# Kernel optimization log

Measured on AMD Instinct MI355X. Metric: run time of the kernel, lower is better.

## Reference

```python
import jax, jax.numpy as jnp
import numpy as np

DIM = 2048
N_HEADS = 16
N_KV_HEADS = 4
HEAD_DIM = DIM // N_HEADS


def setup_inputs() -> dict:
    key = jax.random.key(0)
    k1, k2, k3, k4, k5 = jax.random.split(key, 5)
    B, T = 2, 2048
    scale = 1.0 / np.sqrt(DIM)
    x = jax.random.normal(k1, (B, T, DIM), dtype=jnp.float32)
    # weights stored as [in, out] so forward is x @ W (same math as nn.Linear)
    Wq = jax.random.normal(k2, (DIM, DIM), dtype=jnp.float32) * scale
    Wk = jax.random.normal(k3, (DIM, N_KV_HEADS * HEAD_DIM), dtype=jnp.float32) * scale
    Wv = jax.random.normal(k4, (DIM, N_KV_HEADS * HEAD_DIM), dtype=jnp.float32) * scale
    Wo = jax.random.normal(k5, (DIM, DIM), dtype=jnp.float32) * scale
    return {"x": x, "Wq": Wq, "Wk": Wk, "Wv": Wv, "Wo": Wo}


def reference(x, Wq, Wk, Wv, Wo):
    B, T, C = x.shape
    G = N_HEADS // N_KV_HEADS  # query heads per kv head
    # projections
    q = (x @ Wq).reshape(B, T, N_KV_HEADS, G, HEAD_DIM)   # [B,T,K,G,d]
    k = (x @ Wk).reshape(B, T, N_KV_HEADS, HEAD_DIM)      # [B,T,K,d]
    v = (x @ Wv).reshape(B, T, N_KV_HEADS, HEAD_DIM)      # [B,T,K,d]
    # attention scores: grouped heads share kv head (no repeat_interleave copy)
    att = jnp.einsum('btkgd,bskd->bkgts', q, k) / np.sqrt(HEAD_DIM)  # [B,K,G,T,T]
    att = jax.nn.softmax(att, axis=-1)
    out = jnp.einsum('bkgts,bskd->btkgd', att, v).reshape(B, T, C)
    return out @ Wo
```

## Files before the change

### kernel.cpp

```cpp
#include <hip/hip_runtime.h>
#include <hip/hip_bf16.h>

typedef __hip_bfloat16 bf16;
typedef __attribute__((ext_vector_type(8))) short short8;
typedef __attribute__((ext_vector_type(4))) short short4v;
typedef __attribute__((ext_vector_type(4))) float f32x4;

#define DIMC 2048
#define TSEQ 2048
#define NB 2
#define KVH 4
#define NH 16
#define HD 128
#define KVD 512
#define QSCALE 0.12751744f

__device__ __forceinline__ void mfma16(f32x4& acc, short8 a, short8 b) {
  acc = __builtin_amdgcn_mfma_f32_16x16x32_bf16(a, b, acc, 0, 0, 0);
}

__device__ __forceinline__ void gload_lds16(const bf16* g, bf16* l) {
  __builtin_amdgcn_global_load_lds(
      (const __attribute__((address_space(1))) void*)g,
      (__attribute__((address_space(3))) void*)l, 16, 0, 0);
}

__device__ __forceinline__ int swz(int row, int col) {
  return col ^ ((row & 7) << 3);
}

__global__ __launch_bounds__(256) void f2b(const float* __restrict__ in,
                                           bf16* __restrict__ out, long n4) {
  long i = (long)blockIdx.x * 256 + threadIdx.x;
  if (i >= n4) return;
  const f32x4 v = *(const f32x4*)(in + i * 4);
  union { short4v s; bf16 h[4]; } u;
#pragma unroll
  for (int j = 0; j < 4; ++j) u.h[j] = __float2bfloat16(v[j]);
  *(short4v*)(out + i * 4) = u.s;
}

__global__ __launch_bounds__(256) void transpose_all(const float* __restrict__ Wq,
                                                     const float* __restrict__ Wk,
                                                     const float* __restrict__ Wv,
                                                     const float* __restrict__ Wo,
                                                     bf16* __restrict__ WT3,
                                                     bf16* __restrict__ WoT) {
  __shared__ bf16 tile[64][72];
  const int y = blockIdx.y;
  const float* in;
  bf16* out;
  int C, rb, cb;
  float scale = 1.0f;
  if (y < 32) {
    in = Wq; out = WT3; C = 2048;
    rb = y * 64; cb = blockIdx.x * 64; scale = QSCALE;
  } else if (y < 40) {
    in = Wk; out = WT3 + (long)2048 * DIMC; C = 512;
    rb = blockIdx.x * 64; cb = (y - 32) * 64;
  } else if (y < 48) {
    in = Wv; out = WT3 + (long)2560 * DIMC; C = 512;
    rb = blockIdx.x * 64; cb = (y - 40) * 64;
  } else {
    in = Wo; out = WoT; C = 2048;
    rb = (y - 48) * 64; cb = blockIdx.x * 64;
  }
  int tx = threadIdx.x & 63, ty = threadIdx.x >> 6;
  for (int i = ty; i < 64; i += 4)
    tile[i][tx] = __float2bfloat16(in[(long)(rb + i) * C + cb + tx] * scale);
  __syncthreads();
  for (int i = ty; i < 64; i += 4)
    out[(long)(cb + i) * DIMC + rb + tx] = tile[tx][i];
}

#define GEMM_BODY(A_, Bt_, K_)                                                  \
  const int tid = threadIdx.x;                                                  \
  const int lane = tid & 63, wid = tid >> 6;                                    \
  const long m0 = blockIdx.y * 128, n0 = blockIdx.x * 128;                      \
  const int wm = (wid >> 1) * 64, wn = (wid & 1) * 64;                          \
  f32x4 acc[4][4] = {};                                                         \
  const int srow = lane >> 2, scol = (lane & 3) * 8;                            \
  const bf16* Ag = A_ + (m0 + srow) * (long)K_ + scol;                          \
  const bf16* Bg = Bt_ + (n0 + srow) * (long)K_ + scol;                         \
  for (int k0 = 0; k0 < K_; k0 += 32) {                                         \
    for (int p = 0; p < 2; ++p) {                                               \
      int rr = p * 64 + wid * 16;                                               \
      gload_lds16(Ag + (long)rr * K_ + k0, As + rr * 32);                       \
      gload_lds16(Bg + (long)rr * K_ + k0, Bs + rr * 32);                       \
    }                                                                           \
    __syncthreads();                                                            \
    const int ko = (lane >> 4) * 8;                                             \
    short8 af[4], bq[4];                                                        \
    _Pragma("unroll") for (int i = 0; i < 4; ++i) {                             \
      af[i] = *(const short8*)(As + (wm + i * 16 + (lane & 15)) * 32 + ko);     \
      bq[i] = *(const short8*)(Bs + (wn + i * 16 + (lane & 15)) * 32 + ko);     \
    }                                                                           \
    _Pragma("unroll") for (int i = 0; i < 4; ++i)                               \
      _Pragma("unroll") for (int j = 0; j < 4; ++j)                             \
        mfma16(acc[i][j], af[i], bq[j]);                                        \
    __syncthreads();                                                            \
  }                                                                             \
  const int cr = (lane >> 4) * 4, cc = lane & 15;

__global__ __launch_bounds__(256) void gemm_qkv(const bf16* __restrict__ A,
                                                const bf16* __restrict__ Bt,
                                                bf16* __restrict__ qp,
                                                bf16* __restrict__ kp,
                                                bf16* __restrict__ vT) {
  __shared__ bf16 As[128 * 32];
  __shared__ bf16 Bs[128 * 32];
  GEMM_BODY(A, Bt, 2048)
#pragma unroll
  for (int i = 0; i < 4; ++i)
#pragma unroll
    for (int j = 0; j < 4; ++j)
#pragma unroll
      for (int r = 0; r < 4; ++r) {
        long m = m0 + wm + i * 16 + cr + r;
        long n = n0 + wn + j * 16 + cc;
        float val = acc[i][j][r];
        if (n0 < 2048) {
          qp[m * DIMC + n] = __float2bfloat16(val);
        } else if (n0 < 2560) {
          kp[m * KVD + (n - 2048)] = __float2bfloat16(val);
        } else {
          long nn = n - 2560;
          long z = (m >> 11) * 4 + (nn >> 7);
          vT[z * (HD * (long)TSEQ) + (nn & 127) * (long)TSEQ + (m & 2047)] =
              __float2bfloat16(val);
        }
      }
}

__global__ __launch_bounds__(256) void gemm_out(const bf16* __restrict__ A,
                                                const bf16* __restrict__ Bt,
                                                float* __restrict__ C) {
  __shared__ bf16 As[128 * 32];
  __shared__ bf16 Bs[128 * 32];
  GEMM_BODY(A, Bt, 2048)
#pragma unroll
  for (int i = 0; i < 4; ++i)
#pragma unroll
    for (int j = 0; j < 4; ++j)
#pragma unroll
      for (int r = 0; r < 4; ++r) {
        long m = m0 + wm + i * 16 + cr + r;
        long n = n0 + wn + j * 16 + cc;
        C[m * DIMC + n] = acc[i][j][r];
      }
}

__global__ __launch_bounds__(512, 2) void attn_fwd(const bf16* __restrict__ Qp,
                                                   const bf16* __restrict__ Kp,
                                                   const bf16* __restrict__ Vt,
                                                   bf16* __restrict__ AO) {
  __shared__ bf16 Ks[2][64 * 128];
  __shared__ bf16 Vts[2][128 * 64];
  const int tid = threadIdx.x;
  const int lane = tid & 63, wid = tid >> 6;
  const int h = blockIdx.y, b = blockIdx.z;
  const int kv = h >> 2;
  const int t0 = blockIdx.x * 256;
  const int lr = lane & 15, lg = lane >> 4;

  short8 aq[2][4];
#pragma unroll
  for (int f = 0; f < 2; ++f) {
    const bf16* qrow =
        Qp + ((long)(b * TSEQ + t0 + wid * 32 + f * 16 + lr)) * DIMC + h * HD + lg * 8;
#pragma unroll
    for (int c = 0; c < 4; ++c) aq[f][c] = *(const short8*)(qrow + c * 32);
  }
  f32x4 o[2][8] = {};
  float mrun[2] = {-1e30f, -1e30f}, lrun[2] = {0.f, 0.f};

  const bf16* Kg = Kp + (long)b * TSEQ * KVD + kv * HD;
  const bf16* Vg = Vt + ((long)(b * KVH + kv)) * HD * TSEQ;

  const int krow = tid >> 3, kc0 = (tid & 7) * 16;
  const int vrow = tid >> 2, va = tid & 3;
  short8 kreg[2], vreg[2];
#pragma unroll
  for (int p = 0; p < 2; ++p) {
    kreg[p] = *(const short8*)(Kg + (long)krow * KVD + kc0 + p * 8);
    vreg[p] = *(const short8*)(Vg + (long)vrow * TSEQ + (va * 16 + 8 * p));
  }

  for (int s0 = 0; s0 < TSEQ; s0 += 64) {
    const int buf = (s0 >> 6) & 1;
    bf16* Kb = Ks[buf];
    bf16* Vb = Vts[buf];
#pragma unroll
    for (int p = 0; p < 2; ++p) {
      *(short8*)(Kb + krow * 128 + swz(krow, kc0 + p * 8)) = kreg[p];
      union { short8 s; short4v q[2]; } u;
      u.s = vreg[p];
      int sl1 = (4 * (va >> 1) + 2 * p + vrow) & 7;
      int sl2 = (4 * (va >> 1) + 2 * p + 1 + vrow) & 7;
      int hf = (va & 1) * 4;
      *(short4v*)(Vb + vrow * 64 + sl1 * 8 + hf) = u.q[0];
      *(short4v*)(Vb + vrow * 64 + sl2 * 8 + hf) = u.q[1];
    }
    __syncthreads();
    if (s0 + 64 < TSEQ) {
#pragma unroll
      for (int p = 0; p < 2; ++p) {
        kreg[p] = *(const short8*)(Kg + (long)(s0 + 64 + krow) * KVD + kc0 + p * 8);
        vreg[p] = *(const short8*)(Vg + (long)vrow * TSEQ + s0 + 64 + (va * 16 + 8 * p));
      }
    }

    f32x4 sacc[2][4] = {};
    __builtin_amdgcn_s_setprio(1);
#pragma unroll
    for (int sf = 0; sf < 4; ++sf)
#pragma unroll
      for (int c = 0; c < 4; ++c) {
        int row = sf * 16 + lr;
        short8 kf = *(const short8*)(Kb + row * 128 + swz(row, c * 32 + lg * 8));
        mfma16(sacc[0][sf], kf, aq[0][c]);
        mfma16(sacc[1][sf], kf, aq[1][c]);
      }
    __builtin_amdgcn_s_setprio(0);

    union { short8 s; bf16 h[8]; } pb[2][2];
#pragma unroll
    for (int f = 0; f < 2; ++f) {
      float tmax = sacc[f][0][0];
#pragma unroll
      for (int sf = 0; sf < 4; ++sf)
#pragma unroll
        for (int r = 0; r < 4; ++r) tmax = fmaxf(tmax, sacc[f][sf][r]);
      tmax = fmaxf(tmax, __shfl_xor(tmax, 16));
      tmax = fmaxf(tmax, __shfl_xor(tmax, 32));
      if (__any(tmax > mrun[f] + 8.0f)) {
        float mnew = fmaxf(mrun[f], tmax);
        float fac = exp2f(mrun[f] - mnew);
        mrun[f] = mnew;
        lrun[f] *= fac;
#pragma unroll
        for (int df = 0; df < 8; ++df) o[f][df] *= fac;
      }
      float p4[4][4];
      float ps = 0.f;
#pragma unroll
      for (int sf = 0; sf < 4; ++sf)
#pragma unroll
        for (int r = 0; r < 4; ++r) {
          float pv = exp2f(sacc[f][sf][r] - mrun[f]);
          p4[sf][r] = pv;
          ps += pv;
        }
      ps += __shfl_xor(ps, 16);
      ps += __shfl_xor(ps, 32);
      lrun[f] += ps;
#pragma unroll
      for (int c2 = 0; c2 < 2; ++c2)
#pragma unroll
        for (int r = 0; r < 4; ++r) {
          pb[f][c2].h[r] = __float2bfloat16(p4[2 * c2][r]);
          pb[f][c2].h[4 + r] = __float2bfloat16(p4[2 * c2 + 1][r]);
        }
    }

    __builtin_amdgcn_s_setprio(1);
#pragma unroll
    for (int c2 = 0; c2 < 2; ++c2) {
#pragma unroll
      for (int df = 0; df < 8; ++df) {
        int row = df * 16 + lr;
        short8 vf = *(const short8*)(Vb + row * 64 + ((4 * c2 + lg + row) & 7) * 8);
        mfma16(o[0][df], vf, pb[0][c2].s);
        mfma16(o[1][df], vf, pb[1][c2].s);
      }
    }
    __builtin_amdgcn_s_setprio(0);
  }

#pragma unroll
  for (int f = 0; f < 2; ++f) {
    float inv = 1.0f / lrun[f];
    bf16* obase =
        AO + ((long)(b * TSEQ + t0 + wid * 32 + f * 16 + lr)) * DIMC + h * HD + lg * 4;
#pragma unroll
    for (int df = 0; df < 8; ++df) {
      union { short4v s; bf16 h[4]; } ov;
#pragma unroll
      for (int r = 0; r < 4; ++r) ov.h[r] = __float2bfloat16(o[f][df][r] * inv);
      *(short4v*)(obase + df * 16) = ov.s;
    }
  }
}

extern "C" void kernel_launch(void* const* d_in, const int* in_sizes, int n_in,
                              void* d_out, int out_size, void* d_ws, size_t ws_size,
                              hipStream_t stream) {
  const float* x  = (const float*)d_in[0];
  const float* Wq = (const float*)d_in[1];
  const float* Wk = (const float*)d_in[2];
  const float* Wv = (const float*)d_in[3];
  const float* Wo = (const float*)d_in[4];
  float* out = (float*)d_out;
  bf16* ws = (bf16*)d_ws;

  bf16* xb  = ws;
  bf16* WT3 = xb + 8388608;
  bf16* WoT = WT3 + 6291456;
  bf16* qp  = WoT + 4194304;
  bf16* kp  = qp + 8388608;
  bf16* vT  = kp + 2097152;

  f2b<<<8192, 256, 0, stream>>>(x, xb, 2097152);
  transpose_all<<<dim3(32, 80), 256, 0, stream>>>(Wq, Wk, Wv, Wo, WT3, WoT);

  gemm_qkv<<<dim3(24, 32), 256, 0, stream>>>(xb, WT3, qp, kp, vT);

  bf16* ao = xb;
  attn_fwd<<<dim3(8, 16, 2), 512, 0, stream>>>(qp, kp, vT, ao);

  gemm_out<<<dim3(16, 32), 256, 0, stream>>>(ao, WoT, out);
}
```

Before: 232.4 us.

## Halve attention block size to 128 queries and use native exp2 intrinsic

The attention kernel now runs 256-thread blocks covering 128 query rows instead of 512-thread blocks covering 256, which doubles the grid to 512 blocks for better CU coverage. Each thread now loads twice as many K/V chunks into LDS per tile to keep the cooperative load complete. exp2f is also replaced with the raw hardware exp2 builtin where available, dropping range handling. The trade-off is that K/V tiles are loaded twice as often per query, which adds memory traffic, along with slightly different exp precision behavior.

```diff
diff --git a/kernel.cpp b/kernel.cpp
--- a/kernel.cpp
+++ b/kernel.cpp
@@ -14,6 +14,12 @@
 #define HD 128
 #define KVD 512
 #define QSCALE 0.12751744f
+
+#if __has_builtin(__builtin_amdgcn_exp2f)
+#define EXP2(x) __builtin_amdgcn_exp2f(x)
+#else
+#define EXP2(x) exp2f(x)
+#endif
 
 __device__ __forceinline__ void mfma16(f32x4& acc, short8 a, short8 b) {
   acc = __builtin_amdgcn_mfma_f32_16x16x32_bf16(a, b, acc, 0, 0, 0);
@@ -150,7 +156,7 @@
       }
 }
 
-__global__ __launch_bounds__(512, 2) void attn_fwd(const bf16* __restrict__ Qp,
+__global__ __launch_bounds__(256, 2) void attn_fwd(const bf16* __restrict__ Qp,
                                                    const bf16* __restrict__ Kp,
                                                    const bf16* __restrict__ Vt,
                                                    bf16* __restrict__ AO) {
@@ -160,7 +166,7 @@
   const int lane = tid & 63, wid = tid >> 6;
   const int h = blockIdx.y, b = blockIdx.z;
   const int kv = h >> 2;
-  const int t0 = blockIdx.x * 256;
+  const int t0 = blockIdx.x * 128;
   const int lr = lane & 15, lg = lane >> 4;
 
   short8 aq[2][4];
@@ -177,37 +183,47 @@
   const bf16* Kg = Kp + (long)b * TSEQ * KVD + kv * HD;
   const bf16* Vg = Vt + ((long)(b * KVH + kv)) * HD * TSEQ;
 
-  const int krow = tid >> 3, kc0 = (tid & 7) * 16;
-  const int vrow = tid >> 2, va = tid & 3;
-  short8 kreg[2], vreg[2];
-#pragma unroll
-  for (int p = 0; p < 2; ++p) {
-    kreg[p] = *(const short8*)(Kg + (long)krow * KVD + kc0 + p * 8);
-    vreg[p] = *(const short8*)(Vg + (long)vrow * TSEQ + (va * 16 + 8 * p));
-  }
+  const int krow = tid >> 2;
+  const int vrow = tid >> 1;
+  short8 kreg[2][2], vreg[2][2];
+#pragma unroll
+  for (int s = 0; s < 2; ++s)
+#pragma unroll
+    for (int p = 0; p < 2; ++p) {
+      kreg[s][p] = *(const short8*)(Kg + (long)krow * KVD + (2 * (tid & 3) + s) * 16 + p * 8);
+      vreg[s][p] = *(const short8*)(Vg + (long)vrow * TSEQ + (2 * (tid & 1) + s) * 16 + 8 * p);
+    }
 
   for (int s0 = 0; s0 < TSEQ; s0 += 64) {
     const int buf = (s0 >> 6) & 1;
     bf16* Kb = Ks[buf];
     bf16* Vb = Vts[buf];
 #pragma unroll
-    for (int p = 0; p < 2; ++p) {
-      *(short8*)(Kb + krow * 128 + swz(krow, kc0 + p * 8)) = kreg[p];
-      union { short8 s; short4v q[2]; } u;
-      u.s = vreg[p];
-      int sl1 = (4 * (va >> 1) + 2 * p + vrow) & 7;
-      int sl2 = (4 * (va >> 1) + 2 * p + 1 + vrow) & 7;
-      int hf = (va & 1) * 4;
-      *(short4v*)(Vb + vrow * 64 + sl1 * 8 + hf) = u.q[0];
-      *(short4v*)(Vb + vrow * 64 + sl2 * 8 + hf) = u.q[1];
-    }
+    for (int s = 0; s < 2; ++s)
+#pragma unroll
+      for (int p = 0; p < 2; ++p) {
+        int kc0 = (2 * (tid & 3) + s) * 16;
+        *(short8*)(Kb + krow * 128 + swz(krow, kc0 + p * 8)) = kreg[s][p];
+        int va = 2 * (tid & 1) + s;
+        union { short8 v8; short4v q[2]; } u;
+        u.v8 = vreg[s][p];
+        int sl1 = (4 * (va >> 1) + 2 * p + vrow) & 7;
+        int sl2 = (4 * (va >> 1) + 2 * p + 1 + vrow) & 7;
+        int hf = (va & 1) * 4;
+        *(short4v*)(Vb + vrow * 64 + sl1 * 8 + hf) = u.q[0];
+        *(short4v*)(Vb + vrow * 64 + sl2 * 8 + hf) = u.q[1];
+      }
     __syncthreads();
     if (s0 + 64 < TSEQ) {
 #pragma unroll
-      for (int p = 0; p < 2; ++p) {
-        kreg[p] = *(const short8*)(Kg + (long)(s0 + 64 + krow) * KVD + kc0 + p * 8);
-        vreg[p] = *(const short8*)(Vg + (long)vrow * TSEQ + s0 + 64 + (va * 16 + 8 * p));
-      }
+      for (int s = 0; s < 2; ++s)
+#pragma unroll
+        for (int p = 0; p < 2; ++p) {
+          kreg[s][p] = *(const short8*)(Kg + (long)(s0 + 64 + krow) * KVD +
+                                        (2 * (tid & 3) + s) * 16 + p * 8);
+          vreg[s][p] = *(const short8*)(Vg + (long)vrow * TSEQ + s0 + 64 +
+                                        (2 * (tid & 1) + s) * 16 + 8 * p);
+        }
     }
 
     f32x4 sacc[2][4] = {};
@@ -235,7 +251,7 @@
       tmax = fmaxf(tmax, __shfl_xor(tmax, 32));
       if (__any(tmax > mrun[f] + 8.0f)) {
         float mnew = fmaxf(mrun[f], tmax);
-        float fac = exp2f(mrun[f] - mnew);
+        float fac = EXP2(mrun[f] - mnew);
         mrun[f] = mnew;
         lrun[f] *= fac;
 #pragma unroll
@@ -247,7 +263,7 @@
       for (int sf = 0; sf < 4; ++sf)
 #pragma unroll
         for (int r = 0; r < 4; ++r) {
-          float pv = exp2f(sacc[f][sf][r] - mrun[f]);
+          float pv = EXP2(sacc[f][sf][r] - mrun[f]);
           p4[sf][r] = pv;
           ps += pv;
         }
@@ -316,7 +332,7 @@
   gemm_qkv<<<dim3(24, 32), 256, 0, stream>>>(xb, WT3, qp, kp, vT);
 
   bf16* ao = xb;
-  attn_fwd<<<dim3(8, 16, 2), 512, 0, stream>>>(qp, kp, vT, ao);
+  attn_fwd<<<dim3(16, 16, 2), 256, 0, stream>>>(qp, kp, vT, ao);
 
   gemm_out<<<dim3(16, 32), 256, 0, stream>>>(ao, WoT, out);
 }
```

Result: faster. 226.6 us (-2.5%).

## Split attention over two KV halves with a combine kernel and smaller tiles

Applied to the files above, without the earlier changes.

The attention kernel now splits the key/value sequence into two halves handled by separate blocks. Each block emits unnormalised partial outputs plus running max and sum, and a new combine kernel merges the two halves with a log-sum-exp rescale. Blocks shrink to 256 threads and 128 query rows with 32-key tiles, and exp2 uses the AMDGCN builtin. The aim is four times as many blocks to fill the GPU better; the cost is a second kernel pass over a larger bf16 intermediate and more barriers per unit of work.

```diff
diff --git a/kernel.cpp b/kernel.cpp
--- a/kernel.cpp
+++ b/kernel.cpp
@@ -14,6 +14,12 @@
 #define HD 128
 #define KVD 512
 #define QSCALE 0.12751744f
+
+#if __has_builtin(__builtin_amdgcn_exp2f)
+#define EXP2(x) __builtin_amdgcn_exp2f(x)
+#else
+#define EXP2(x) exp2f(x)
+#endif
 
 __device__ __forceinline__ void mfma16(f32x4& acc, short8 a, short8 b) {
   acc = __builtin_amdgcn_mfma_f32_16x16x32_bf16(a, b, acc, 0, 0, 0);
@@ -150,17 +156,21 @@
       }
 }
 
-__global__ __launch_bounds__(512, 2) void attn_fwd(const bf16* __restrict__ Qp,
+__global__ __launch_bounds__(256, 2) void attn_fwd(const bf16* __restrict__ Qp,
                                                    const bf16* __restrict__ Kp,
                                                    const bf16* __restrict__ Vt,
-                                                   bf16* __restrict__ AO) {
-  __shared__ bf16 Ks[2][64 * 128];
-  __shared__ bf16 Vts[2][128 * 64];
+                                                   bf16* __restrict__ op2,
+                                                   float* __restrict__ mlb) {
+  __shared__ bf16 Ks[2][32 * 128];
+  __shared__ bf16 Vts[2][128 * 32];
   const int tid = threadIdx.x;
   const int lane = tid & 63, wid = tid >> 6;
-  const int h = blockIdx.y, b = blockIdx.z;
+  const int h = blockIdx.y;
+  const int z = blockIdx.z;
+  const int b = z & 1, half = z >> 1;
+  const int s_lo = half * 1024, s_hi = s_lo + 1024;
   const int kv = h >> 2;
-  const int t0 = blockIdx.x * 256;
+  const int t0 = blockIdx.x * 128;
   const int lr = lane & 15, lg = lane >> 4;
 
   short8 aq[2][4];
@@ -178,42 +188,40 @@
   const bf16* Vg = Vt + ((long)(b * KVH + kv)) * HD * TSEQ;
 
   const int krow = tid >> 3, kc0 = (tid & 7) * 16;
-  const int vrow = tid >> 2, va = tid & 3;
+  const int vrow = tid >> 1, va = tid & 1;
   short8 kreg[2], vreg[2];
 #pragma unroll
   for (int p = 0; p < 2; ++p) {
-    kreg[p] = *(const short8*)(Kg + (long)krow * KVD + kc0 + p * 8);
-    vreg[p] = *(const short8*)(Vg + (long)vrow * TSEQ + (va * 16 + 8 * p));
-  }
-
-  for (int s0 = 0; s0 < TSEQ; s0 += 64) {
-    const int buf = (s0 >> 6) & 1;
+    kreg[p] = *(const short8*)(Kg + (long)(s_lo + krow) * KVD + kc0 + p * 8);
+    vreg[p] = *(const short8*)(Vg + (long)vrow * TSEQ + s_lo + va * 16 + 8 * p);
+  }
+
+  for (int s0 = s_lo; s0 < s_hi; s0 += 32) {
+    const int buf = (s0 >> 5) & 1;
     bf16* Kb = Ks[buf];
     bf16* Vb = Vts[buf];
 #pragma unroll
     for (int p = 0; p < 2; ++p) {
       *(short8*)(Kb + krow * 128 + swz(krow, kc0 + p * 8)) = kreg[p];
-      union { short8 s; short4v q[2]; } u;
-      u.s = vreg[p];
-      int sl1 = (4 * (va >> 1) + 2 * p + vrow) & 7;
-      int sl2 = (4 * (va >> 1) + 2 * p + 1 + vrow) & 7;
-      int hf = (va & 1) * 4;
-      *(short4v*)(Vb + vrow * 64 + sl1 * 8 + hf) = u.q[0];
-      *(short4v*)(Vb + vrow * 64 + sl2 * 8 + hf) = u.q[1];
+      union { short8 v8; short4v q[2]; } u;
+      u.v8 = vreg[p];
+      int q1 = (2 * p + vrow) & 3, q2 = (2 * p + 1 + vrow) & 3;
+      *(short4v*)(Vb + vrow * 32 + q1 * 8 + va * 4) = u.q[0];
+      *(short4v*)(Vb + vrow * 32 + q2 * 8 + va * 4) = u.q[1];
     }
     __syncthreads();
-    if (s0 + 64 < TSEQ) {
+    if (s0 + 32 < s_hi) {
 #pragma unroll
       for (int p = 0; p < 2; ++p) {
-        kreg[p] = *(const short8*)(Kg + (long)(s0 + 64 + krow) * KVD + kc0 + p * 8);
-        vreg[p] = *(const short8*)(Vg + (long)vrow * TSEQ + s0 + 64 + (va * 16 + 8 * p));
-      }
-    }
-
-    f32x4 sacc[2][4] = {};
+        kreg[p] = *(const short8*)(Kg + (long)(s0 + 32 + krow) * KVD + kc0 + p * 8);
+        vreg[p] = *(const short8*)(Vg + (long)vrow * TSEQ + s0 + 32 + va * 16 + 8 * p);
+      }
+    }
+
+    f32x4 sacc[2][2] = {};
     __builtin_amdgcn_s_setprio(1);
 #pragma unroll
-    for (int sf = 0; sf < 4; ++sf)
+    for (int sf = 0; sf < 2; ++sf)
 #pragma unroll
       for (int c = 0; c < 4; ++c) {
         int row = sf * 16 + lr;
@@ -223,73 +231,90 @@
       }
     __builtin_amdgcn_s_setprio(0);
 
-    union { short8 s; bf16 h[8]; } pb[2][2];
+    union { short8 s; bf16 h[8]; } pb[2];
 #pragma unroll
     for (int f = 0; f < 2; ++f) {
       float tmax = sacc[f][0][0];
 #pragma unroll
-      for (int sf = 0; sf < 4; ++sf)
+      for (int sf = 0; sf < 2; ++sf)
 #pragma unroll
         for (int r = 0; r < 4; ++r) tmax = fmaxf(tmax, sacc[f][sf][r]);
       tmax = fmaxf(tmax, __shfl_xor(tmax, 16));
       tmax = fmaxf(tmax, __shfl_xor(tmax, 32));
       if (__any(tmax > mrun[f] + 8.0f)) {
         float mnew = fmaxf(mrun[f], tmax);
-        float fac = exp2f(mrun[f] - mnew);
+        float fac = EXP2(mrun[f] - mnew);
         mrun[f] = mnew;
         lrun[f] *= fac;
 #pragma unroll
         for (int df = 0; df < 8; ++df) o[f][df] *= fac;
       }
-      float p4[4][4];
       float ps = 0.f;
 #pragma unroll
-      for (int sf = 0; sf < 4; ++sf)
-#pragma unroll
-        for (int r = 0; r < 4; ++r) {
-          float pv = exp2f(sacc[f][sf][r] - mrun[f]);
-          p4[sf][r] = pv;
-          ps += pv;
-        }
+      for (int r = 0; r < 4; ++r) {
+        float v0 = EXP2(sacc[f][0][r] - mrun[f]);
+        float v1 = EXP2(sacc[f][1][r] - mrun[f]);
+        ps += v0 + v1;
+        pb[f].h[r] = __float2bfloat16(v0);
+        pb[f].h[4 + r] = __float2bfloat16(v1);
+      }
       ps += __shfl_xor(ps, 16);
       ps += __shfl_xor(ps, 32);
       lrun[f] += ps;
-#pragma unroll
-      for (int c2 = 0; c2 < 2; ++c2)
-#pragma unroll
-        for (int r = 0; r < 4; ++r) {
-          pb[f][c2].h[r] = __float2bfloat16(p4[2 * c2][r]);
-          pb[f][c2].h[4 + r] = __float2bfloat16(p4[2 * c2 + 1][r]);
-        }
     }
 
     __builtin_amdgcn_s_setprio(1);
 #pragma unroll
-    for (int c2 = 0; c2 < 2; ++c2) {
-#pragma unroll
-      for (int df = 0; df < 8; ++df) {
-        int row = df * 16 + lr;
-        short8 vf = *(const short8*)(Vb + row * 64 + ((4 * c2 + lg + row) & 7) * 8);
-        mfma16(o[0][df], vf, pb[0][c2].s);
-        mfma16(o[1][df], vf, pb[1][c2].s);
-      }
+    for (int df = 0; df < 8; ++df) {
+      int row = df * 16 + lr;
+      short8 vf = *(const short8*)(Vb + row * 32 + ((lg + row) & 3) * 8);
+      mfma16(o[0][df], vf, pb[0].s);
+      mfma16(o[1][df], vf, pb[1].s);
     }
     __builtin_amdgcn_s_setprio(0);
   }
 
 #pragma unroll
   for (int f = 0; f < 2; ++f) {
-    float inv = 1.0f / lrun[f];
-    bf16* obase =
-        AO + ((long)(b * TSEQ + t0 + wid * 32 + f * 16 + lr)) * DIMC + h * HD + lg * 4;
+    int t = t0 + wid * 32 + f * 16 + lr;
+    bf16* obase = op2 + ((long)z * TSEQ + t) * DIMC + h * HD + lg * 4;
 #pragma unroll
     for (int df = 0; df < 8; ++df) {
       union { short4v s; bf16 h[4]; } ov;
 #pragma unroll
-      for (int r = 0; r < 4; ++r) ov.h[r] = __float2bfloat16(o[f][df][r] * inv);
+      for (int r = 0; r < 4; ++r) ov.h[r] = __float2bfloat16(o[f][df][r]);
       *(short4v*)(obase + df * 16) = ov.s;
     }
-  }
+    if (lg == 0) {
+      long mi = ((long)z * TSEQ + t) * NH + h;
+      mlb[mi] = mrun[f];
+      mlb[(long)4 * TSEQ * NH + mi] = lrun[f];
+    }
+  }
+}
+
+__global__ __launch_bounds__(256) void attn_combine(bf16* __restrict__ op2,
+                                                    const float* __restrict__ mlb) {
+  long idx = (long)blockIdx.x * 256 + threadIdx.x;
+  int r = idx >> 8, c8 = idx & 255;
+  int b = r >> 11, t = r & 2047, h = c8 >> 4;
+  long z1 = b, z2 = 2 + b;
+  long m1i = (z1 * TSEQ + t) * NH + h, m2i = (z2 * TSEQ + t) * NH + h;
+  const long loff = (long)4 * TSEQ * NH;
+  float m1 = mlb[m1i], m2 = mlb[m2i];
+  float l1 = mlb[loff + m1i], l2 = mlb[loff + m2i];
+  float m = fmaxf(m1, m2);
+  float a1 = EXP2(m1 - m), a2 = EXP2(m2 - m);
+  float inv = 1.0f / (l1 * a1 + l2 * a2);
+  a1 *= inv; a2 *= inv;
+  union { short8 s; bf16 h[8]; } o1, o2, ov;
+  o1.s = *(const short8*)(op2 + (z1 * TSEQ + t) * DIMC + c8 * 8);
+  o2.s = *(const short8*)(op2 + (z2 * TSEQ + t) * DIMC + c8 * 8);
+#pragma unroll
+  for (int j = 0; j < 8; ++j)
+    ov.h[j] = __float2bfloat16(__bfloat162float(o1.h[j]) * a1 +
+                               __bfloat162float(o2.h[j]) * a2);
+  *(short8*)(op2 + (z1 * TSEQ + t) * DIMC + c8 * 8) = ov.s;
 }
 
 extern "C" void kernel_launch(void* const* d_in, const int* in_sizes, int n_in,
@@ -303,20 +328,24 @@
   float* out = (float*)d_out;
   bf16* ws = (bf16*)d_ws;
 
-  bf16* xb  = ws;
-  bf16* WT3 = xb + 8388608;
-  bf16* WoT = WT3 + 6291456;
-  bf16* qp  = WoT + 4194304;
-  bf16* kp  = qp + 8388608;
-  bf16* vT  = kp + 2097152;
+  bf16* xb    = ws;
+  bf16* WT3   = xb + 8388608;
+  bf16* spare = WT3 + 6291456;
+  bf16* WoT   = spare + 2097152;
+  bf16* qp    = WoT + 4194304;
+  bf16* kp    = qp + 8388608;
+  bf16* vT    = kp + 2097152;
+  float* mlb  = (float*)(vT + 2097152);
+  bf16* op2   = xb;
+  bf16* ao    = op2;
 
   f2b<<<8192, 256, 0, stream>>>(x, xb, 2097152);
   transpose_all<<<dim3(32, 80), 256, 0, stream>>>(Wq, Wk, Wv, Wo, WT3, WoT);
 
   gemm_qkv<<<dim3(24, 32), 256, 0, stream>>>(xb, WT3, qp, kp, vT);
 
-  bf16* ao = xb;
-  attn_fwd<<<dim3(8, 16, 2), 512, 0, stream>>>(qp, kp, vT, ao);
+  attn_fwd<<<dim3(16, 16, 4), 256, 0, stream>>>(qp, kp, vT, op2, mlb);
+  attn_combine<<<4096, 256, 0, stream>>>(op2, mlb);
 
   gemm_out<<<dim3(16, 32), 256, 0, stream>>>(ao, WoT, out);
 }
```

Result: slower. 248.4 us (+6.9%).
